# Kernel optimization log

Measured on AMD Instinct MI355X. Metric: run time of the kernel, lower is better.

The kernel has to match this reference:

```python
import jax, jax.numpy as jnp
import numpy as np

INPUT_SIZE = 64
HIDDEN_SIZE = 256
NUM_CLASSES = 10
BATCH = 512
SEQ_LEN = 1024


def setup_inputs() -> dict:
    key = jax.random.key(0)
    ks = jax.random.split(key, 6)
    std = 1.0 / np.sqrt(HIDDEN_SIZE)
    x = jax.random.normal(ks[0], (BATCH, SEQ_LEN, INPUT_SIZE), dtype=jnp.float32)
    # GRUCell params (reset_parameters: uniform(-std, std))
    Wx = jax.random.uniform(ks[1], (3 * HIDDEN_SIZE, INPUT_SIZE), minval=-std, maxval=std, dtype=jnp.float32)
    Wh = jax.random.uniform(ks[2], (3 * HIDDEN_SIZE, HIDDEN_SIZE), minval=-std, maxval=std, dtype=jnp.float32)
    bias = jax.random.uniform(ks[3], (3 * HIDDEN_SIZE,), minval=-std, maxval=std, dtype=jnp.float32)
    # fc: Linear(hidden_size, num_classes), default torch init ~ uniform(-1/sqrt(H), 1/sqrt(H))
    fc_w = jax.random.uniform(ks[4], (NUM_CLASSES, HIDDEN_SIZE), minval=-std, maxval=std, dtype=jnp.float32)
    fc_b = jax.random.uniform(ks[5], (NUM_CLASSES,), minval=-std, maxval=std, dtype=jnp.float32)
    return {"x": x, "Wx": Wx, "Wh": Wh, "bias": bias, "fc_w": fc_w, "fc_b": fc_b}


def reference(x, Wx, Wh, bias, fc_w, fc_b):
    B, S, _ = x.shape
    H = Wh.shape[1]
    b_r, b_z, b_h = jnp.split(bias, 3)
    # Precompute input gates for all timesteps in one GEMM: [B, S, 3H]
    gate_x = jnp.einsum('bsi,gi->bsg', x, Wx)

    def step(h, gx_t):
        gate_h = h @ Wh.T  # [B, 3H]
        i_r, i_z, i_h = jnp.split(gx_t, 3, axis=1)
        h_r, h_z, h_h = jnp.split(gate_h, 3, axis=1)
        reset_gate = jax.nn.sigmoid(i_r + h_r + b_r)
        update_gate = jax.nn.sigmoid(i_z + h_z + b_z)
        new_gate = jnp.tanh(i_h + reset_gate * h_h + b_h)
        hy = new_gate + update_gate * (h - new_gate)
        return hy, None

    h0 = jnp.zeros((B, H), dtype=x.dtype)
    hT, _ = jax.lax.scan(step, h0, jnp.swapaxes(gate_x, 0, 1))  # scan over time
    logit = hT @ fc_w.T + fc_b
    return logit
```

## Files before the change

### kernel.cpp

```cpp
#include <hip/hip_runtime.h>


typedef short v8s __attribute__((ext_vector_type(8)));
typedef float f32x4 __attribute__((ext_vector_type(4)));

#define LOG2E 1.4426950408889634f

__device__ __forceinline__ unsigned short f2b(float f) {
    unsigned int u = __float_as_uint(f);
    u += 0x7FFFu + ((u >> 16) & 1u);
    return (unsigned short)(u >> 16);
}
__device__ __forceinline__ float b2f(unsigned short h) {
    return __uint_as_float(((unsigned int)h) << 16);
}
__device__ __forceinline__ v8s cvt8(f32x4 a, f32x4 b) {
    v8s r;
#pragma unroll
    for (int j = 0; j < 4; ++j) { r[j] = (short)f2b(a[j]); r[4 + j] = (short)f2b(b[j]); }
    return r;
}
__device__ __forceinline__ v8s wfrag(const float* src, float s) {
    f32x4 a = *(const f32x4*)src, b = *(const f32x4*)(src + 4);
    a *= s; b *= s;
    return cvt8(a, b);
}
__device__ __forceinline__ float rcpf(float v) {
#if __has_builtin(__builtin_amdgcn_rcpf)
    return __builtin_amdgcn_rcpf(v);
#else
    return 1.0f / v;
#endif
}
__device__ __forceinline__ float exp2f_(float v) {
#if __has_builtin(__builtin_amdgcn_exp2f)
    return __builtin_amdgcn_exp2f(v);
#else
    return __exp2f(v);
#endif
}
__device__ __forceinline__ float sg(float v) { return rcpf(1.0f + exp2f_(-v)); }
__device__ __forceinline__ f32x4 MF(v8s a, v8s b, f32x4 c) {
    return __builtin_amdgcn_mfma_f32_16x16x32_bf16(a, b, c, 0, 0, 0);
}
__device__ __forceinline__ int fidx(int row, int k) {
    return ((k >> 5) << 9) + ((((k >> 3) & 3) << 4) + row) * 8 + (k & 7);
}

#define LDSX_WN   0
#define LDSX_H    131072
#define LDSX_X    147456
#define LDSX_SIZE 151552

extern "C" __global__ void __launch_bounds__(1024, 4)
gru_v10(const float* __restrict__ x, const float* __restrict__ Wx,
        const float* __restrict__ Wh, const float* __restrict__ bias,
        const float* __restrict__ fcw, const float* __restrict__ fcb,
        float* __restrict__ out)
{
    extern __shared__ char lds[];
    v8s* wnl = (v8s*)(lds + LDSX_WN);
    char* hl = lds + LDSX_H;
    char* xl = lds + LDSX_X;

    const int tid = threadIdx.x;
    const int w = tid >> 6, l = tid & 63;
    const int cl = l & 15, kg = l >> 4;
    const int b0 = blockIdx.x << 4;
    const int ch = (w << 4) + cl;

#pragma unroll
    for (int ks = 0; ks < 8; ++ks)
        wnl[(w*8 + ks)*64 + l] =
            wfrag(Wh + (size_t)(512 + ch)*256 + ks*32 + kg*8, 2.0f*LOG2E);

    v8s rW[10], zW[10], nX[2];
#pragma unroll
    for (int ks = 0; ks < 8; ++ks) {
        rW[ks] = wfrag(Wh + (size_t)ch*256 + ks*32 + kg*8, LOG2E);
        zW[ks] = wfrag(Wh + (size_t)(256 + ch)*256 + ks*32 + kg*8, LOG2E);
    }
#pragma unroll
    for (int k2 = 0; k2 < 2; ++k2) {
        rW[8+k2] = wfrag(Wx + (size_t)ch*64 + k2*32 + kg*8, LOG2E);
        zW[8+k2] = wfrag(Wx + (size_t)(256 + ch)*64 + k2*32 + kg*8, LOG2E);
        nX[k2]   = wfrag(Wx + (size_t)(512 + ch)*64 + k2*32 + kg*8, 2.0f*LOG2E);
    }
    const float br = bias[ch] * LOG2E;
    const float bz = bias[256 + ch] * LOG2E;
    const float bn = bias[512 + ch] * (2.0f*LOG2E);

    const int chb = ((ch >> 5) << 9) + (((ch >> 3) & 3) << 7) + (ch & 7);

    for (int i = tid; i < 2048; i += 1024) ((unsigned int*)hl)[i] = 0u;
    float hprev[4] = {0, 0, 0, 0};

    const int xr = tid >> 6, xc = tid & 63;
    const int xidx = fidx(xr, xc);
    {
        float v = x[((size_t)(b0 + xr) * 1024 + 0) * 64 + xc];
        *(unsigned short*)(xl + xidx*2) = f2b(v);
    }

    for (int t = 0; t < 1024; ++t) {
        __syncthreads();
        const int cur = t & 1;
        const v8s* hb = (const v8s*)(hl + cur * 8192);
        const v8s* xb = (const v8s*)(xl + cur * 2048);

        float xv = 0.0f;
        if (t < 1023)
            xv = x[((size_t)(b0 + xr) * 1024 + (t + 1)) * 64 + xc];

        f32x4 aR = {br, br, br, br};
        f32x4 aZ = {bz, bz, bz, bz};
        f32x4 aNh = {0, 0, 0, 0};
        f32x4 aNx = {bn, bn, bn, bn};

#pragma unroll
        for (int ks = 0; ks < 8; ++ks) {
            v8s a  = hb[(ks << 6) + l];
            v8s nW = wnl[(w*8 + ks)*64 + l];
            aR  = MF(a, rW[ks], aR);
            aZ  = MF(a, zW[ks], aZ);
            aNh = MF(a, nW, aNh);
        }
#pragma unroll
        for (int k2 = 0; k2 < 2; ++k2) {
            v8s ax = xb[(k2 << 6) + l];
            aR  = MF(ax, rW[8+k2], aR);
            aZ  = MF(ax, zW[8+k2], aZ);
            aNx = MF(ax, nX[k2], aNx);
        }

        unsigned short* hn = (unsigned short*)(hl + (cur ^ 1) * 8192);
#pragma unroll
        for (int i = 0; i < 4; ++i) {
            float rg = sg(aR[i]);
            float zg = sg(aZ[i]);
            float nv = __builtin_fmaf(rg, aNh[i], aNx[i]);
            float ng = __builtin_fmaf(2.0f, sg(nv), -1.0f);
            float hy = ng + zg * (hprev[i] - ng);
            hprev[i] = hy;
            hn[chb + ((kg << 2) + i) * 8] = f2b(hy);
        }
        if (t < 1023)
            *(unsigned short*)(xl + (cur ^ 1) * 2048 + xidx*2) = f2b(xv);
    }

    __syncthreads();
    const unsigned short* hf = (const unsigned short*)hl;
    if (tid < 160) {
        int row = tid / 10, cls = tid - row * 10;
        float s = fcb[cls];
        const float* wrow = fcw + cls * 256;
        for (int k = 0; k < 256; ++k)
            s += b2f(hf[fidx(row, k)]) * wrow[k];
        out[(b0 + row) * 10 + cls] = s;
    }
}

extern "C" void kernel_launch(void* const* d_in, const int* in_sizes, int n_in,
                              void* d_out, int out_size, void* d_ws, size_t ws_size,
                              hipStream_t stream) {
    const float* x    = (const float*)d_in[0];
    const float* Wx   = (const float*)d_in[1];
    const float* Wh   = (const float*)d_in[2];
    const float* bias = (const float*)d_in[3];
    const float* fcw  = (const float*)d_in[4];
    const float* fcb  = (const float*)d_in[5];
    (void)d_ws; (void)ws_size;

    (void)hipFuncSetAttribute((const void*)gru_v10,
                              hipFuncAttributeMaxDynamicSharedMemorySize, LDSX_SIZE);
    gru_v10<<<dim3(32), dim3(1024), LDSX_SIZE, stream>>>(
        x, Wx, Wh, bias, fcw, fcb, (float*)d_out);
}
```

Measured before the change: 1.995 ms.

## Halve block to 512 threads, keep all Wh in registers, chunk input projection

Each wave now owns two 16-channel tiles per gate, so all three Wh gate blocks live in registers instead of the new-gate block being read from LDS every step. The input projection is moved out of the per-step MFMA chain: every 4 timesteps the x slice is loaded and projected, and the gate pre-activations are stored in LDS as fp16 and read back per step. The aim is fewer LDS reads on the serial recurrence and a shorter critical path per step. In exchange, register pressure is much higher, Wx fragments are reloaded from global memory every chunk, fp16 rounding is added to the input gates, and the x load for each chunk is no longer hidden behind the previous step.

```diff
diff --git a/kernel.cpp b/kernel.cpp
--- a/kernel.cpp
+++ b/kernel.cpp
@@ -1,10 +1,21 @@
 #include <hip/hip_runtime.h>
+#include <hip/hip_fp16.h>
 
 
 typedef short v8s __attribute__((ext_vector_type(8)));
 typedef float f32x4 __attribute__((ext_vector_type(4)));
+typedef unsigned int u32x4 __attribute__((ext_vector_type(4)));
 
 #define LOG2E 1.4426950408889634f
+#define CHUNK 4
+#define NCH   256
+#define REC   48
+#define GXT   (512 * REC)
+
+#define L_H    0
+#define L_XF   16384
+#define L_GX   24576
+#define LDS_SZ 122880
 
 __device__ __forceinline__ unsigned short f2b(float f) {
     unsigned int u = __float_as_uint(f);
@@ -13,6 +24,14 @@
 }
 __device__ __forceinline__ float b2f(unsigned short h) {
     return __uint_as_float(((unsigned int)h) << 16);
+}
+__device__ __forceinline__ unsigned int pkh(float a, float b) {
+    return (unsigned int)__half_as_ushort(__float2half_rn(a))
+         | ((unsigned int)__half_as_ushort(__float2half_rn(b)) << 16);
+}
+__device__ __forceinline__ float hxu(unsigned int u, int hi) {
+    unsigned short b = (unsigned short)(hi ? (u >> 16) : (u & 0xFFFFu));
+    return __half2float(__ushort_as_half(b));
 }
 __device__ __forceinline__ v8s cvt8(f32x4 a, f32x4 b) {
     v8s r;
@@ -47,105 +66,127 @@
     return ((k >> 5) << 9) + ((((k >> 3) & 3) << 4) + row) * 8 + (k & 7);
 }
 
-#define LDSX_WN   0
-#define LDSX_H    131072
-#define LDSX_X    147456
-#define LDSX_SIZE 151552
-
-extern "C" __global__ void __launch_bounds__(1024, 4)
-gru_v10(const float* __restrict__ x, const float* __restrict__ Wx,
+extern "C" __global__ void __launch_bounds__(512, 2)
+gru_v12(const float* __restrict__ x, const float* __restrict__ Wx,
         const float* __restrict__ Wh, const float* __restrict__ bias,
         const float* __restrict__ fcw, const float* __restrict__ fcb,
         float* __restrict__ out)
 {
     extern __shared__ char lds[];
-    v8s* wnl = (v8s*)(lds + LDSX_WN);
-    char* hl = lds + LDSX_H;
-    char* xl = lds + LDSX_X;
+    char* hl = lds + L_H;
+    unsigned short* xf = (unsigned short*)(lds + L_XF);
+    char* gxl = lds + L_GX;
 
     const int tid = threadIdx.x;
     const int w = tid >> 6, l = tid & 63;
     const int cl = l & 15, kg = l >> 4;
     const int b0 = blockIdx.x << 4;
-    const int ch = (w << 4) + cl;
-
-#pragma unroll
-    for (int ks = 0; ks < 8; ++ks)
-        wnl[(w*8 + ks)*64 + l] =
-            wfrag(Wh + (size_t)(512 + ch)*256 + ks*32 + kg*8, 2.0f*LOG2E);
-
-    v8s rW[10], zW[10], nX[2];
-#pragma unroll
-    for (int ks = 0; ks < 8; ++ks) {
-        rW[ks] = wfrag(Wh + (size_t)ch*256 + ks*32 + kg*8, LOG2E);
-        zW[ks] = wfrag(Wh + (size_t)(256 + ch)*256 + ks*32 + kg*8, LOG2E);
+    const int tiles[6] = {2*w, 2*w+1, 16+2*w, 17+2*w, 32+2*w, 33+2*w};
+
+    v8s whB[6][8];
+#pragma unroll
+    for (int tt = 0; tt < 6; ++tt) {
+        const float sc = (tt < 4) ? LOG2E : 2.0f * LOG2E;
+        const float* src = Wh + (size_t)(tiles[tt] * 16 + cl) * 256 + kg * 8;
+#pragma unroll
+        for (int ks = 0; ks < 8; ++ks)
+            whB[tt][ks] = wfrag(src + ks * 32, sc);
     }
-#pragma unroll
-    for (int k2 = 0; k2 < 2; ++k2) {
-        rW[8+k2] = wfrag(Wx + (size_t)ch*64 + k2*32 + kg*8, LOG2E);
-        zW[8+k2] = wfrag(Wx + (size_t)(256 + ch)*64 + k2*32 + kg*8, LOG2E);
-        nX[k2]   = wfrag(Wx + (size_t)(512 + ch)*64 + k2*32 + kg*8, 2.0f*LOG2E);
-    }
-    const float br = bias[ch] * LOG2E;
-    const float bz = bias[256 + ch] * LOG2E;
-    const float bn = bias[512 + ch] * (2.0f*LOG2E);
-
-    const int chb = ((ch >> 5) << 9) + (((ch >> 3) & 3) << 7) + (ch & 7);
-
-    for (int i = tid; i < 2048; i += 1024) ((unsigned int*)hl)[i] = 0u;
-    float hprev[4] = {0, 0, 0, 0};
-
-    const int xr = tid >> 6, xc = tid & 63;
-    const int xidx = fidx(xr, xc);
-    {
-        float v = x[((size_t)(b0 + xr) * 1024 + 0) * 64 + xc];
-        *(unsigned short*)(xl + xidx*2) = f2b(v);
-    }
-
-    for (int t = 0; t < 1024; ++t) {
+    float bv6[6];
+#pragma unroll
+    for (int tt = 0; tt < 6; ++tt)
+        bv6[tt] = bias[tiles[tt] * 16 + cl] * ((tt < 4) ? LOG2E : 2.0f * LOG2E);
+
+    for (int i = tid; i < 2048; i += 512) ((unsigned int*)hl)[i] = 0u;
+    float hprev[8] = {0, 0, 0, 0, 0, 0, 0, 0};
+
+    const int a_tl = tid >> 7;
+    const int a_rm = tid & 127;
+    const int a_r  = a_rm >> 3;
+    const int a_k0 = (a_rm & 7) << 3;
+    unsigned short* const a_dst = xf + a_tl * 1024 + fidx(a_r, a_k0);
+    const float* const a_src = x + (size_t)(b0 + a_r) * 65536 + a_k0;
+
+    char* const my_rec = gxl + tid * REC;
+    const int chbase0 = ((w << 5) + cl);
+
+    for (int c = 0; c < NCH; ++c) {
+        const int c0 = c << 2;
+
+        {
+            const float* xs = a_src + (size_t)(c0 + a_tl) * 64;
+            *(v8s*)a_dst = cvt8(*(const f32x4*)xs, *(const f32x4*)(xs + 4));
+        }
         __syncthreads();
-        const int cur = t & 1;
-        const v8s* hb = (const v8s*)(hl + cur * 8192);
-        const v8s* xb = (const v8s*)(xl + cur * 2048);
-
-        float xv = 0.0f;
-        if (t < 1023)
-            xv = x[((size_t)(b0 + xr) * 1024 + (t + 1)) * 64 + xc];
-
-        f32x4 aR = {br, br, br, br};
-        f32x4 aZ = {bz, bz, bz, bz};
-        f32x4 aNh = {0, 0, 0, 0};
-        f32x4 aNx = {bn, bn, bn, bn};
-
-#pragma unroll
-        for (int ks = 0; ks < 8; ++ks) {
-            v8s a  = hb[(ks << 6) + l];
-            v8s nW = wnl[(w*8 + ks)*64 + l];
-            aR  = MF(a, rW[ks], aR);
-            aZ  = MF(a, zW[ks], aZ);
-            aNh = MF(a, nW, aNh);
+
+#pragma unroll
+        for (int ps = 0; ps < 3; ++ps) {
+            const float sc = (ps < 2) ? LOG2E : 2.0f * LOG2E;
+            const int ta = tiles[ps * 2], tb = tiles[ps * 2 + 1];
+            const float* wsa = Wx + (size_t)(ta * 16 + cl) * 64 + kg * 8;
+            const float* wsb = Wx + (size_t)(tb * 16 + cl) * 64 + kg * 8;
+            v8s wa0 = wfrag(wsa, sc), wa1 = wfrag(wsa + 32, sc);
+            v8s wb0 = wfrag(wsb, sc), wb1 = wfrag(wsb + 32, sc);
+            const float ba = bv6[ps * 2], bb = bv6[ps * 2 + 1];
+            const v8s* xv = (const v8s*)xf;
+#pragma unroll
+            for (int tl = 0; tl < CHUNK; ++tl) {
+                v8s a0 = xv[tl * 128 + l];
+                v8s a1 = xv[tl * 128 + 64 + l];
+                f32x4 aa = {ba, ba, ba, ba}, ab = {bb, bb, bb, bb};
+                aa = MF(a0, wa0, aa); aa = MF(a1, wa1, aa);
+                ab = MF(a0, wb0, ab); ab = MF(a1, wb1, ab);
+                u32x4 s = {pkh(aa[0], aa[1]), pkh(aa[2], aa[3]),
+                           pkh(ab[0], ab[1]), pkh(ab[2], ab[3])};
+                *(u32x4*)(my_rec + tl * GXT + ps * 16) = s;
+            }
         }
-#pragma unroll
-        for (int k2 = 0; k2 < 2; ++k2) {
-            v8s ax = xb[(k2 << 6) + l];
-            aR  = MF(ax, rW[8+k2], aR);
-            aZ  = MF(ax, zW[8+k2], aZ);
-            aNx = MF(ax, nX[k2], aNx);
+
+#pragma unroll
+        for (int tl = 0; tl < CHUNK; ++tl) {
+            const int t = c0 + tl;
+            __syncthreads();
+            const int cur = t & 1;
+            const v8s* hb = (const v8s*)(hl + cur * 8192);
+
+            const u32x4* gq = (const u32x4*)(my_rec + tl * GXT);
+            u32x4 gr = gq[0], gz = gq[1], gn = gq[2];
+
+            f32x4 aR[2], aZ[2], aN[2];
+            aR[0] = f32x4{0, 0, 0, 0}; aR[1] = f32x4{0, 0, 0, 0};
+            aZ[0] = f32x4{0, 0, 0, 0}; aZ[1] = f32x4{0, 0, 0, 0};
+            aN[0] = f32x4{0, 0, 0, 0}; aN[1] = f32x4{0, 0, 0, 0};
+
+#pragma unroll
+            for (int ks = 0; ks < 8; ++ks) {
+                v8s a = hb[(ks << 6) + l];
+                aR[0] = MF(a, whB[0][ks], aR[0]);
+                aR[1] = MF(a, whB[1][ks], aR[1]);
+                aZ[0] = MF(a, whB[2][ks], aZ[0]);
+                aZ[1] = MF(a, whB[3][ks], aZ[1]);
+                aN[0] = MF(a, whB[4][ks], aN[0]);
+                aN[1] = MF(a, whB[5][ks], aN[1]);
+            }
+
+            unsigned short* hn = (unsigned short*)(hl + (cur ^ 1) * 8192);
+#pragma unroll
+            for (int p = 0; p < 2; ++p) {
+                const int ch = chbase0 + (p << 4);
+                const int chbase = ((ch >> 5) << 9) + (((ch >> 3) & 3) << 7) + (ch & 7);
+#pragma unroll
+                for (int i = 0; i < 4; ++i) {
+                    const int dw = p * 2 + (i >> 1), hi = i & 1;
+                    float rg = sg(aR[p][i] + hxu(gr[dw], hi));
+                    float zg = sg(aZ[p][i] + hxu(gz[dw], hi));
+                    float nv = __builtin_fmaf(rg, aN[p][i], hxu(gn[dw], hi));
+                    float ng = __builtin_fmaf(2.0f, sg(nv), -1.0f);
+                    float hy = ng + zg * (hprev[p * 4 + i] - ng);
+                    hprev[p * 4 + i] = hy;
+                    hn[chbase + ((kg << 2) + i) * 8] = f2b(hy);
+                }
+            }
         }
-
-        unsigned short* hn = (unsigned short*)(hl + (cur ^ 1) * 8192);
-#pragma unroll
-        for (int i = 0; i < 4; ++i) {
-            float rg = sg(aR[i]);
-            float zg = sg(aZ[i]);
-            float nv = __builtin_fmaf(rg, aNh[i], aNx[i]);
-            float ng = __builtin_fmaf(2.0f, sg(nv), -1.0f);
-            float hy = ng + zg * (hprev[i] - ng);
-            hprev[i] = hy;
-            hn[chb + ((kg << 2) + i) * 8] = f2b(hy);
-        }
-        if (t < 1023)
-            *(unsigned short*)(xl + (cur ^ 1) * 2048 + xidx*2) = f2b(xv);
+        __syncthreads();
     }
 
     __syncthreads();
@@ -171,8 +212,8 @@
     const float* fcb  = (const float*)d_in[5];
     (void)d_ws; (void)ws_size;
 
-    (void)hipFuncSetAttribute((const void*)gru_v10,
-                              hipFuncAttributeMaxDynamicSharedMemorySize, LDSX_SIZE);
-    gru_v10<<<dim3(32), dim3(1024), LDSX_SIZE, stream>>>(
+    (void)hipFuncSetAttribute((const void*)gru_v12,
+                              hipFuncAttributeMaxDynamicSharedMemorySize, LDS_SZ);
+    gru_v12<<<dim3(32), dim3(512), LDS_SZ, stream>>>(
         x, Wx, Wh, bias, fcw, fcb, (float*)d_out);
 }
```

New measurement: 2.995 ms. +50.1%, slower.
